# Kernel tuning notes

Measured on AMD Instinct MI355X. Metric: run time of the kernel, lower is better.

Reference implementation:

```python
import jax, jax.numpy as jnp
import numpy as np

B, S, E, H = 16, 512, 768, 12
D = E // H
SCALING = 1.0 / np.sqrt(D * 1.0)  # scaling_factor = 1


def setup_inputs() -> dict:
    key = jax.random.key(0)
    ks = jax.random.split(key, 8)
    query = jax.random.normal(ks[0], (B, S, E), dtype=jnp.float32)
    key_in = jax.random.normal(ks[1], (B, S, E), dtype=jnp.float32)
    value = jax.random.normal(ks[2], (B, S, E), dtype=jnp.float32)
    key_padding_mask = jax.random.randint(ks[3], (B, S), 0, 2).astype(jnp.bool_)
    attn_bias = jax.random.normal(ks[4], (B, H, S, S), dtype=jnp.float32)
    # Learned params. NOTE: original code applies wq to q, k AND v (wk/wv unused).
    Wq = jax.random.normal(ks[5], (E, E), dtype=jnp.float32) * (1.0 / np.sqrt(E))
    bq = jnp.zeros((E,), dtype=jnp.float32)
    Wo = jax.random.normal(ks[6], (E, E), dtype=jnp.float32) * (1.0 / np.sqrt(E))
    bo = jnp.zeros((E,), dtype=jnp.float32)
    return {"query": query, "key": key_in, "value": value,
            "key_padding_mask": key_padding_mask, "attn_bias": attn_bias,
            "Wq": Wq, "bq": bq, "Wo": Wo, "bo": bo}


def _split_heads(x):
    # [B,S,E] -> [B,H,S,D]
    return x.reshape(B, S, H, D).transpose(0, 2, 1, 3)


def reference(query, key, value, key_padding_mask, attn_bias, Wq, bq, Wo, bo):
    q = (query @ Wq + bq) * jnp.asarray(SCALING, query.dtype)
    k = key @ Wq + bq      # faithful: wq used for k and v in the source
    v = value @ Wq + bq
    q, k, v = _split_heads(q), _split_heads(k), _split_heads(v)  # [B,H,S,D]
    w = jnp.einsum('bhtd,bhsd->bhts', q, k)                      # [B,H,T,S]
    w = jnp.where(key_padding_mask[:, None, None, :], -jnp.inf, w)
    w = w + attn_bias
    attn = jax.nn.softmax(w, axis=-1)  # dropout is no-op (training=False)
    o = jnp.einsum('bhts,bhsd->bhtd', attn, v)
    o = o.transpose(0, 2, 1, 3).reshape(B, S, E)
    o = o @ Wo + bo
    attn_weights = w.reshape(B * H, S, S)
    return (o, attn_weights, attn.reshape(B * H, S, S))
```

## Files before the change

### kernel.cpp

```cpp
#include <hip/hip_runtime.h>
#include <cmath>

#define BB 16
#define SS 512
#define EE 768
#define HH 12
#define DD 64
#define NBH (BB*HH)

#define MASK_NEG (-1.0e30f)

__device__ __forceinline__ unsigned short bf16_rn(float x) {
    unsigned u = __float_as_uint(x);
    u += 0x7FFFu + ((u >> 16) & 1u);
    return (unsigned short)(u >> 16);
}
__device__ __forceinline__ float bf16_tof(unsigned short h) {
    return __uint_as_float(((unsigned)h) << 16);
}

typedef __attribute__((ext_vector_type(8))) short bf16x8;
typedef __attribute__((ext_vector_type(4))) float f32x4;
typedef __attribute__((ext_vector_type(4))) unsigned short u16x4;

__global__ __launch_bounds__(256) void conv_w_kernel(
    const float* __restrict__ Wq, const float* __restrict__ Wo,
    unsigned short* __restrict__ wtq, unsigned short* __restrict__ wto)
{
    const float* __restrict__ W = blockIdx.z ? Wo : Wq;
    unsigned short* __restrict__ wt = blockIdx.z ? wto : wtq;
    const int k = blockIdx.x * 256 + threadIdx.x;
    const int n = blockIdx.y;
    const float x = W[(size_t)k * EE + n];
    const unsigned short h = bf16_rn(x);
    const float r = x - bf16_tof(h);
    const unsigned short m = bf16_rn(r);
    const float l2 = r - bf16_tof(m);
    const unsigned short l = bf16_rn(l2);
    const size_t PL = (size_t)EE * EE;
    wt[0 * PL + (size_t)n * EE + k] = h;
    wt[1 * PL + (size_t)n * EE + k] = m;
    wt[2 * PL + (size_t)n * EE + k] = l;
}

__global__ __launch_bounds__(256) void split_gemm_qkv_kernel(
    const float* __restrict__ Xq, const float* __restrict__ Xk,
    const float* __restrict__ Xv, const unsigned short* __restrict__ wt,
    const float* __restrict__ bvec,
    unsigned short* __restrict__ qp, unsigned short* __restrict__ kp,
    unsigned short* __restrict__ vtp)
{
    const int z = blockIdx.z;
    const float* __restrict__ X = (z == 1) ? Xk : (z == 2) ? Xv : Xq;
    const float scale = (z == 0) ? 0.125f : 1.0f;

    const int m0 = blockIdx.x * 128;
    const int n0 = blockIdx.y * 128;

    __shared__ __align__(16) unsigned short lds[4 * 4096];
    const int AH = 0, AL = 4096, BH = 8192, BL = 12288;

    const int tid = threadIdx.x;
    const int srow = tid >> 2;
    const int sg   = tid & 3;
    const int wv = tid >> 6;
    const int wr = wv >> 1, wc = wv & 1;
    const int lane = tid & 63;
    const int l15 = lane & 15, lg = lane >> 4;

    const size_t PL = (size_t)EE * EE;
    const size_t PS = (size_t)NBH * SS * DD;

    f32x4 acc[4][4];
#pragma unroll
    for (int i = 0; i < 4; ++i)
#pragma unroll
        for (int j = 0; j < 4; ++j) acc[i][j] = (f32x4){0.f, 0.f, 0.f, 0.f};

    float4 xf[2][2];
    bf16x8 wh[2], wl[2];

#define QKV_LOAD(K0)                                                          \
    {                                                                         \
        _Pragma("unroll")                                                     \
        for (int half = 0; half < 2; ++half) {                                \
            const int row = srow + 64 * half;                                 \
            const float* xp = &X[(size_t)(m0 + row) * EE + (K0) + sg * 8];    \
            xf[half][0] = *reinterpret_cast<const float4*>(xp);               \
            xf[half][1] = *reinterpret_cast<const float4*>(xp + 4);           \
            const size_t bo = (size_t)(n0 + row) * EE + (K0) + sg * 8;        \
            wh[half] = *reinterpret_cast<const bf16x8*>(&wt[0 * PL + bo]);    \
            wl[half] = *reinterpret_cast<const bf16x8*>(&wt[1 * PL + bo]);    \
        }                                                                     \
    }

    QKV_LOAD(0);

#pragma unroll 1
    for (int k0 = 0; k0 < EE; k0 += 32) {
        __syncthreads();
#pragma unroll
        for (int half = 0; half < 2; ++half) {
            const int row = srow + 64 * half;
            const float xs[8] = {xf[half][0].x, xf[half][0].y, xf[half][0].z, xf[half][0].w,
                                 xf[half][1].x, xf[half][1].y, xf[half][1].z, xf[half][1].w};
            bf16x8 hv, mv;
#pragma unroll
            for (int e = 0; e < 8; ++e) {
                const float x = xs[e];
                const unsigned short h = bf16_rn(x);
                const unsigned short m = bf16_rn(x - bf16_tof(h));
                hv[e] = (short)h;
                mv[e] = (short)m;
            }
            const int o = row * 32 + sg * 8;
            *reinterpret_cast<bf16x8*>(&lds[AH + o]) = hv;
            *reinterpret_cast<bf16x8*>(&lds[AL + o]) = mv;
            *reinterpret_cast<bf16x8*>(&lds[BH + o]) = wh[half];
            *reinterpret_cast<bf16x8*>(&lds[BL + o]) = wl[half];
        }
        __syncthreads();

        if (k0 + 32 < EE) QKV_LOAD(k0 + 32);

        bf16x8 ah[4], al[4];
#pragma unroll
        for (int i = 0; i < 4; ++i) {
            const int o = (wr * 64 + i * 16 + l15) * 32 + lg * 8;
            ah[i] = *reinterpret_cast<const bf16x8*>(&lds[AH + o]);
            al[i] = *reinterpret_cast<const bf16x8*>(&lds[AL + o]);
        }
#pragma unroll
        for (int j = 0; j < 4; ++j) {
            const int o = (wc * 64 + j * 16 + l15) * 32 + lg * 8;
            const bf16x8 bh = *reinterpret_cast<const bf16x8*>(&lds[BH + o]);
            const bf16x8 bl = *reinterpret_cast<const bf16x8*>(&lds[BL + o]);
#pragma unroll
            for (int i = 0; i < 4; ++i) {
                acc[i][j] = __builtin_amdgcn_mfma_f32_16x16x32_bf16(ah[i], bh, acc[i][j], 0, 0, 0);
                acc[i][j] = __builtin_amdgcn_mfma_f32_16x16x32_bf16(ah[i], bl, acc[i][j], 0, 0, 0);
                acc[i][j] = __builtin_amdgcn_mfma_f32_16x16x32_bf16(al[i], bh, acc[i][j], 0, 0, 0);
                acc[i][j] = __builtin_amdgcn_mfma_f32_16x16x32_bf16(al[i], bl, acc[i][j], 0, 0, 0);
            }
        }
    }
#undef QKV_LOAD

    unsigned short* __restrict__ dstp = (z == 0) ? qp : kp;
#pragma unroll
    for (int j = 0; j < 4; ++j) {
        const int n = n0 + wc * 64 + j * 16 + l15;
        const float bvn = bvec[n];
        const int h = n >> 6, d = n & 63;
#pragma unroll
        for (int i = 0; i < 4; ++i) {
            const int mb = m0 + wr * 64 + i * 16 + lg * 4;
#pragma unroll
            for (int r = 0; r < 4; ++r) {
                const int m = mb + r;
                const int bh_ = (m >> 9) * HH + h;
                const int srow_ = m & 511;
                const float val = (acc[i][j][r] + bvn) * scale;
                const unsigned short hi = bf16_rn(val);
                const unsigned short lo = bf16_rn(val - bf16_tof(hi));
                if (z == 2) {
                    const size_t o = ((size_t)bh_ * DD + d) * SS + srow_;
                    vtp[o] = hi;
                    vtp[o + PS] = lo;
                } else {
                    const size_t o = ((size_t)bh_ * SS + srow_) * DD + d;
                    dstp[o] = hi;
                    dstp[o + PS] = lo;
                }
            }
        }
    }
}

__global__ __launch_bounds__(256) void flash_attn_kernel(
    const unsigned short* __restrict__ qp, const unsigned short* __restrict__ kp,
    const unsigned short* __restrict__ vt, const unsigned char* __restrict__ mask,
    const float* __restrict__ bias, float* __restrict__ wout,
    float* __restrict__ ohb, float* __restrict__ stat_m,
    float* __restrict__ stat_inv)
{
    const int p = blockIdx.x;
    const int g = p >> 3;
    const int bh = (p & 7) * 24 + (g >> 3);
    const int t0 = (g & 7) * 64;
    const int b = bh / HH, h = bh % HH;
    const int tid = threadIdx.x;
    const int wv = tid >> 6;
    const int lane = tid & 63, l15 = lane & 15, lg = lane >> 4;
    const size_t PS = (size_t)NBH * SS * DD;

    __shared__ __align__(16) unsigned short kbuf[2 * 64 * 68];
    __shared__ __align__(16) unsigned short vbuf[2 * 64 * 68];
    __shared__ __align__(16) unsigned short pbuf[4 * 2 * 16 * 68];

    bf16x8 bqh[2], bql[2];
    {
        const unsigned short* qbase = &qp[((size_t)bh * SS + t0 + wv * 16) * DD];
#pragma unroll
        for (int kc = 0; kc < 2; ++kc) {
            const size_t o = (size_t)l15 * DD + kc * 32 + lg * 8;
            bqh[kc] = *reinterpret_cast<const bf16x8*>(&qbase[o]);
            bql[kc] = *reinterpret_cast<const bf16x8*>(&qbase[o + PS]);
        }
    }

    float rm = -3.0e38f, rs = 0.0f;

    f32x4 oac[4];
#pragma unroll
    for (int j = 0; j < 4; ++j) oac[j] = (f32x4){0.f, 0.f, 0.f, 0.f};

    const int t = t0 + wv * 16 + l15;

    const unsigned short* __restrict__ kb0 = &kp[(size_t)bh * SS * DD];
    const unsigned short* __restrict__ vb0 = &vt[(size_t)bh * DD * SS];
    const int srow2 = tid >> 3, sg2 = (tid & 7) * 8;

    bf16x8 krh[2], krl[2], vrh[2], vrl[2];

#define FA_LOADKV(SC)                                                         \
    {                                                                         \
        _Pragma("unroll")                                                     \
        for (int rep = 0; rep < 2; ++rep) {                                   \
            const int row = srow2 + rep * 32;                                 \
            krh[rep] = *reinterpret_cast<const bf16x8*>(                      \
                &kb0[(size_t)((SC) + row) * DD + sg2]);                       \
            krl[rep] = *reinterpret_cast<const bf16x8*>(                      \
                &kb0[(size_t)((SC) + row) * DD + sg2 + PS]);                  \
            vrh[rep] = *reinterpret_cast<const bf16x8*>(                      \
                &vb0[(size_t)row * SS + (SC) + sg2]);                         \
            vrl[rep] = *reinterpret_cast<const bf16x8*>(                      \
                &vb0[(size_t)row * SS + (SC) + sg2 + PS]);                    \
        }                                                                     \
    }

    FA_LOADKV(0);

#pragma unroll 1
    for (int c = 0; c < 8; ++c) {
        const int sc = c * 64;
        __syncthreads();

#pragma unroll
        for (int rep = 0; rep < 2; ++rep) {
            const int row = srow2 + rep * 32;
            *reinterpret_cast<bf16x8*>(&kbuf[row * 68 + sg2]) = krh[rep];
            *reinterpret_cast<bf16x8*>(&kbuf[64 * 68 + row * 68 + sg2]) = krl[rep];
            *reinterpret_cast<bf16x8*>(&vbuf[row * 68 + sg2]) = vrh[rep];
            *reinterpret_cast<bf16x8*>(&vbuf[64 * 68 + row * 68 + sg2]) = vrl[rep];
        }
        __syncthreads();

        if (c < 7) FA_LOADKV(sc + 64);

        float4 bvr[4];
        uchar4 mkr[4];
#pragma unroll
        for (int i = 0; i < 4; ++i) {
            const int s = sc + i * 16 + lg * 4;
            bvr[i] = *reinterpret_cast<const float4*>(&bias[((size_t)bh * SS + t) * SS + s]);
            mkr[i] = *reinterpret_cast<const uchar4*>(&mask[b * SS + s]);
        }

        f32x4 ws[4];
#pragma unroll
        for (int i = 0; i < 4; ++i) ws[i] = (f32x4){0.f, 0.f, 0.f, 0.f};
#pragma unroll
        for (int kc = 0; kc < 2; ++kc) {
#pragma unroll
            for (int i = 0; i < 4; ++i) {
                const int o = (i * 16 + l15) * 68 + kc * 32 + lg * 8;
                const bf16x8 ah = *reinterpret_cast<const bf16x8*>(&kbuf[o]);
                const bf16x8 al = *reinterpret_cast<const bf16x8*>(&kbuf[64 * 68 + o]);
                ws[i] = __builtin_amdgcn_mfma_f32_16x16x32_bf16(ah, bqh[kc], ws[i], 0, 0, 0);
                ws[i] = __builtin_amdgcn_mfma_f32_16x16x32_bf16(ah, bql[kc], ws[i], 0, 0, 0);
                ws[i] = __builtin_amdgcn_mfma_f32_16x16x32_bf16(al, bqh[kc], ws[i], 0, 0, 0);
                ws[i] = __builtin_amdgcn_mfma_f32_16x16x32_bf16(al, bql[kc], ws[i], 0, 0, 0);
            }
        }

        float mx = -3.0e38f;
#pragma unroll
        for (int i = 0; i < 4; ++i) {
            const int s = sc + i * 16 + lg * 4;
            const size_t go = ((size_t)bh * SS + t) * SS + s;
            float4 w4;
            w4.x = mkr[i].x ? MASK_NEG : ws[i][0] + bvr[i].x;
            w4.y = mkr[i].y ? MASK_NEG : ws[i][1] + bvr[i].y;
            w4.z = mkr[i].z ? MASK_NEG : ws[i][2] + bvr[i].z;
            w4.w = mkr[i].w ? MASK_NEG : ws[i][3] + bvr[i].w;
            *reinterpret_cast<float4*>(&wout[go]) = w4;
            ws[i][0] = w4.x; ws[i][1] = w4.y; ws[i][2] = w4.z; ws[i][3] = w4.w;
            mx = fmaxf(mx, fmaxf(fmaxf(w4.x, w4.y), fmaxf(w4.z, w4.w)));
        }
        mx = fmaxf(mx, __shfl_xor(mx, 16));
        mx = fmaxf(mx, __shfl_xor(mx, 32));

        const float m_new = fmaxf(rm, mx);
        float sm = 0.0f;
#pragma unroll
        for (int i = 0; i < 4; ++i)
#pragma unroll
            for (int r = 0; r < 4; ++r) sm += __expf(ws[i][r] - m_new);
        sm += __shfl_xor(sm, 16);
        sm += __shfl_xor(sm, 32);
        const float scl = __expf(rm - m_new);
        rs = rs * scl + sm;
        rm = m_new;

        unsigned short* pw = &pbuf[(wv * 2) * 16 * 68];
#pragma unroll
        for (int i = 0; i < 4; ++i) {
            float4 p4;
            p4.x = __expf(ws[i][0] - m_new);
            p4.y = __expf(ws[i][1] - m_new);
            p4.z = __expf(ws[i][2] - m_new);
            p4.w = __expf(ws[i][3] - m_new);
            u16x4 hv, lv;
            hv.x = bf16_rn(p4.x); lv.x = bf16_rn(p4.x - bf16_tof(hv.x));
            hv.y = bf16_rn(p4.y); lv.y = bf16_rn(p4.y - bf16_tof(hv.y));
            hv.z = bf16_rn(p4.z); lv.z = bf16_rn(p4.z - bf16_tof(hv.z));
            hv.w = bf16_rn(p4.w); lv.w = bf16_rn(p4.w - bf16_tof(hv.w));
            const int po = l15 * 68 + i * 16 + lg * 4;
            *reinterpret_cast<u16x4*>(&pw[po]) = hv;
            *reinterpret_cast<u16x4*>(&pw[16 * 68 + po]) = lv;
        }

        float sclr[4];
#pragma unroll
        for (int r = 0; r < 4; ++r) sclr[r] = __shfl(scl, lg * 4 + r);
#pragma unroll
        for (int j = 0; j < 4; ++j)
#pragma unroll
            for (int r = 0; r < 4; ++r) oac[j][r] *= sclr[r];

#pragma unroll
        for (int kc = 0; kc < 2; ++kc) {
            const int ko = kc * 32 + lg * 8;
            const bf16x8 pah = *reinterpret_cast<const bf16x8*>(&pw[l15 * 68 + ko]);
            const bf16x8 pal = *reinterpret_cast<const bf16x8*>(&pw[16 * 68 + l15 * 68 + ko]);
#pragma unroll
            for (int j = 0; j < 4; ++j) {
                const int o = (j * 16 + l15) * 68 + ko;
                const bf16x8 vh = *reinterpret_cast<const bf16x8*>(&vbuf[o]);
                const bf16x8 vl = *reinterpret_cast<const bf16x8*>(&vbuf[64 * 68 + o]);
                oac[j] = __builtin_amdgcn_mfma_f32_16x16x32_bf16(pah, vh, oac[j], 0, 0, 0);
                oac[j] = __builtin_amdgcn_mfma_f32_16x16x32_bf16(pah, vl, oac[j], 0, 0, 0);
                oac[j] = __builtin_amdgcn_mfma_f32_16x16x32_bf16(pal, vh, oac[j], 0, 0, 0);
                oac[j] = __builtin_amdgcn_mfma_f32_16x16x32_bf16(pal, vl, oac[j], 0, 0, 0);
            }
        }
    }
#undef FA_LOADKV

    const float inv = 1.0f / rs;
    if (lg == 0) {
        stat_m[(size_t)bh * SS + t] = rm;
        stat_inv[(size_t)bh * SS + t] = inv;
    }
    float invr[4];
#pragma unroll
    for (int r = 0; r < 4; ++r) invr[r] = __shfl(inv, lg * 4 + r);
#pragma unroll
    for (int j = 0; j < 4; ++j)
#pragma unroll
        for (int r = 0; r < 4; ++r) {
            const int tr = t0 + wv * 16 + lg * 4 + r;
            ohb[((size_t)b * SS + tr) * EE + h * DD + j * 16 + l15] = oac[j][r] * invr[r];
        }
}

__global__ __launch_bounds__(256) void finish_kernel(
    const float* __restrict__ X, const unsigned short* __restrict__ wt,
    const float* __restrict__ bvec, float* __restrict__ dflat,
    const float* __restrict__ win, const float* __restrict__ stat_m,
    const float* __restrict__ stat_inv, float* __restrict__ attn)
{
    __shared__ __align__(16) unsigned short lds[4 * 4096];

    if (blockIdx.x >= 384) {
        const int nb = gridDim.x - 384;
        const size_t total = (size_t)NBH * SS * (SS / 4);
        for (size_t g = (size_t)(blockIdx.x - 384) * 256 + threadIdx.x; g < total;
             g += (size_t)nb * 256) {
            const size_t row = g >> 7;
            const float m_ = stat_m[row];
            const float iv = stat_inv[row];
            const float4 w4 = reinterpret_cast<const float4*>(win)[g];
            float4 p4;
            p4.x = __expf(w4.x - m_) * iv;
            p4.y = __expf(w4.y - m_) * iv;
            p4.z = __expf(w4.z - m_) * iv;
            p4.w = __expf(w4.w - m_) * iv;
            reinterpret_cast<float4*>(attn)[g] = p4;
        }
        return;
    }

    const int m0 = (blockIdx.x & 63) * 128;
    const int n0 = (blockIdx.x >> 6) * 128;

    const int AH = 0, AM = 4096, BH = 8192, BM = 12288;

    const int tid = threadIdx.x;
    const int srow = tid >> 2;
    const int sg   = tid & 3;
    const int wv = tid >> 6;
    const int wr = wv >> 1, wc = wv & 1;
    const int lane = tid & 63;
    const int l15 = lane & 15, lg = lane >> 4;
    const size_t PL = (size_t)EE * EE;

    f32x4 acc[4][4];
#pragma unroll
    for (int i = 0; i < 4; ++i)
#pragma unroll
        for (int j = 0; j < 4; ++j) acc[i][j] = (f32x4){0.f, 0.f, 0.f, 0.f};

#pragma unroll 1
    for (int k0 = 0; k0 < EE; k0 += 32) {
#pragma unroll
        for (int half = 0; half < 2; ++half) {
            const int row = srow + 64 * half;
            const float* xp = &X[(size_t)(m0 + row) * EE + k0 + sg * 8];
            const float4 f0 = *reinterpret_cast<const float4*>(xp);
            const float4 f1 = *reinterpret_cast<const float4*>(xp + 4);
            const float xs[8] = {f0.x, f0.y, f0.z, f0.w, f1.x, f1.y, f1.z, f1.w};
            bf16x8 hv, mv;
#pragma unroll
            for (int e = 0; e < 8; ++e) {
                const float x = xs[e];
                const unsigned short h = bf16_rn(x);
                const unsigned short m = bf16_rn(x - bf16_tof(h));
                hv[e] = (short)h;
                mv[e] = (short)m;
            }
            const int o = row * 32 + sg * 8;
            *reinterpret_cast<bf16x8*>(&lds[AH + o]) = hv;
            *reinterpret_cast<bf16x8*>(&lds[AM + o]) = mv;

            const size_t bo = (size_t)(n0 + row) * EE + k0 + sg * 8;
            *reinterpret_cast<bf16x8*>(&lds[BH + o]) =
                *reinterpret_cast<const bf16x8*>(&wt[0 * PL + bo]);
            *reinterpret_cast<bf16x8*>(&lds[BM + o]) =
                *reinterpret_cast<const bf16x8*>(&wt[1 * PL + bo]);
        }
        __syncthreads();

        bf16x8 ah[4], am[4];
#pragma unroll
        for (int i = 0; i < 4; ++i) {
            const int o = (wr * 64 + i * 16 + l15) * 32 + lg * 8;
            ah[i] = *reinterpret_cast<const bf16x8*>(&lds[AH + o]);
            am[i] = *reinterpret_cast<const bf16x8*>(&lds[AM + o]);
        }
#pragma unroll
        for (int j = 0; j < 4; ++j) {
            const int o = (wc * 64 + j * 16 + l15) * 32 + lg * 8;
            const bf16x8 bh = *reinterpret_cast<const bf16x8*>(&lds[BH + o]);
            const bf16x8 bm = *reinterpret_cast<const bf16x8*>(&lds[BM + o]);
#pragma unroll
            for (int i = 0; i < 4; ++i) {
                acc[i][j] = __builtin_amdgcn_mfma_f32_16x16x32_bf16(ah[i], bh, acc[i][j], 0, 0, 0);
                acc[i][j] = __builtin_amdgcn_mfma_f32_16x16x32_bf16(ah[i], bm, acc[i][j], 0, 0, 0);
                acc[i][j] = __builtin_amdgcn_mfma_f32_16x16x32_bf16(am[i], bh, acc[i][j], 0, 0, 0);
                acc[i][j] = __builtin_amdgcn_mfma_f32_16x16x32_bf16(am[i], bm, acc[i][j], 0, 0, 0);
            }
        }
        __syncthreads();
    }

#pragma unroll
    for (int j = 0; j < 4; ++j) {
        const int n = n0 + wc * 64 + j * 16 + l15;
        const float bvn = bvec[n];
#pragma unroll
        for (int i = 0; i < 4; ++i) {
            const int mb = m0 + wr * 64 + i * 16 + lg * 4;
#pragma unroll
            for (int r = 0; r < 4; ++r)
                dflat[(size_t)(mb + r) * EE + n] = acc[i][j][r] + bvn;
        }
    }
}

__global__ __launch_bounds__(256) void proj_kernel(
    const float* __restrict__ Xq, const float* __restrict__ Xk,
    const float* __restrict__ Xv, const float* __restrict__ W,
    const float* __restrict__ bvec, float* __restrict__ qb,
    float* __restrict__ kb, float* __restrict__ vb)
{
    const int z = blockIdx.z;
    const float* __restrict__ X = (z == 0) ? Xq : (z == 1) ? Xk : Xv;
    float* __restrict__ Dst = (z == 0) ? qb : (z == 1) ? kb : vb;
    const float scale = (z == 0) ? 0.125f : 1.0f;

    const int m0 = blockIdx.x * 128;
    const int n0 = blockIdx.y * 128;

    __shared__ float As[16][128];
    __shared__ float Bs[16][128];

    const int tid = threadIdx.x;
    const int ty = tid >> 4, tx = tid & 15;

    float acc[8][8];
#pragma unroll
    for (int i = 0; i < 8; ++i)
#pragma unroll
        for (int j = 0; j < 8; ++j) acc[i][j] = 0.0f;

    const int arow = tid >> 1;
    const int ak   = (tid & 1) * 8;
    const int brow = tid >> 4;
    const int bn   = (tid & 15) * 8;

    for (int k0 = 0; k0 < EE; k0 += 16) {
        const float4* ap = reinterpret_cast<const float4*>(&X[(size_t)(m0 + arow) * EE + k0 + ak]);
        float4 a0 = ap[0], a1 = ap[1];
        As[ak + 0][arow] = a0.x; As[ak + 1][arow] = a0.y;
        As[ak + 2][arow] = a0.z; As[ak + 3][arow] = a0.w;
        As[ak + 4][arow] = a1.x; As[ak + 5][arow] = a1.y;
        As[ak + 6][arow] = a1.z; As[ak + 7][arow] = a1.w;

        const float4* bp = reinterpret_cast<const float4*>(&W[(size_t)(k0 + brow) * EE + n0 + bn]);
        float4 b0 = bp[0], b1 = bp[1];
        *reinterpret_cast<float4*>(&Bs[brow][bn])     = b0;
        *reinterpret_cast<float4*>(&Bs[brow][bn + 4]) = b1;
        __syncthreads();

#pragma unroll
        for (int kk = 0; kk < 16; ++kk) {
            float4 aA = *reinterpret_cast<const float4*>(&As[kk][ty * 8]);
            float4 aB = *reinterpret_cast<const float4*>(&As[kk][ty * 8 + 4]);
            float4 bA = *reinterpret_cast<const float4*>(&Bs[kk][tx * 8]);
            float4 bB = *reinterpret_cast<const float4*>(&Bs[kk][tx * 8 + 4]);
            float av[8] = {aA.x, aA.y, aA.z, aA.w, aB.x, aB.y, aB.z, aB.w};
            float bv[8] = {bA.x, bA.y, bA.z, bA.w, bB.x, bB.y, bB.z, bB.w};
#pragma unroll
            for (int i = 0; i < 8; ++i)
#pragma unroll
                for (int j = 0; j < 8; ++j)
                    acc[i][j] = fmaf(av[i], bv[j], acc[i][j]);
        }
        __syncthreads();
    }

    const int nbase = n0 + tx * 8;
    float bq8[8];
    {
        float4 c0 = *reinterpret_cast<const float4*>(&bvec[nbase]);
        float4 c1 = *reinterpret_cast<const float4*>(&bvec[nbase + 4]);
        bq8[0]=c0.x; bq8[1]=c0.y; bq8[2]=c0.z; bq8[3]=c0.w;
        bq8[4]=c1.x; bq8[5]=c1.y; bq8[6]=c1.z; bq8[7]=c1.w;
    }
    const int hh = nbase >> 6;
    const int dd = nbase & 63;
#pragma unroll
    for (int i = 0; i < 8; ++i) {
        const int m = m0 + ty * 8 + i;
        const int bidx = m >> 9;
        const int srow = m & 511;
        float* dst = &Dst[(((size_t)bidx * HH + hh) * SS + srow) * DD + dd];
        float4 v0, v1;
        v0.x = (acc[i][0] + bq8[0]) * scale;
        v0.y = (acc[i][1] + bq8[1]) * scale;
        v0.z = (acc[i][2] + bq8[2]) * scale;
        v0.w = (acc[i][3] + bq8[3]) * scale;
        v1.x = (acc[i][4] + bq8[4]) * scale;
        v1.y = (acc[i][5] + bq8[5]) * scale;
        v1.z = (acc[i][6] + bq8[6]) * scale;
        v1.w = (acc[i][7] + bq8[7]) * scale;
        *reinterpret_cast<float4*>(dst)     = v0;
        *reinterpret_cast<float4*>(dst + 4) = v1;
    }
}

__global__ __launch_bounds__(256) void scores_kernel(
    const float* __restrict__ qb, const float* __restrict__ kb,
    const unsigned char* __restrict__ mask,
    const float* __restrict__ bias, float* __restrict__ wout)
{
    const int bh = blockIdx.z;
    const int b  = bh / HH;
    const int t0 = blockIdx.y * 128;
    const int s0 = blockIdx.x * 128;

    __shared__ float As[16][128];
    __shared__ float Bs[16][128];

    const int tid = threadIdx.x;
    const int ty = tid >> 4, tx = tid & 15;

    float acc[8][8];
#pragma unroll
    for (int i = 0; i < 8; ++i)
#pragma unroll
        for (int j = 0; j < 8; ++j) acc[i][j] = 0.0f;

    const int arow = tid >> 1;
    const int ak   = (tid & 1) * 8;

    const float* __restrict__ qbase = &qb[(size_t)bh * SS * DD];
    const float* __restrict__ kbase = &kb[(size_t)bh * SS * DD];

    for (int k0 = 0; k0 < DD; k0 += 16) {
        const float4* ap = reinterpret_cast<const float4*>(&qbase[(size_t)(t0 + arow) * DD + k0 + ak]);
        float4 a0 = ap[0], a1 = ap[1];
        As[ak + 0][arow] = a0.x; As[ak + 1][arow] = a0.y;
        As[ak + 2][arow] = a0.z; As[ak + 3][arow] = a0.w;
        As[ak + 4][arow] = a1.x; As[ak + 5][arow] = a1.y;
        As[ak + 6][arow] = a1.z; As[ak + 7][arow] = a1.w;

        const float4* bp = reinterpret_cast<const float4*>(&kbase[(size_t)(s0 + arow) * DD + k0 + ak]);
        float4 b0 = bp[0], b1 = bp[1];
        Bs[ak + 0][arow] = b0.x; Bs[ak + 1][arow] = b0.y;
        Bs[ak + 2][arow] = b0.z; Bs[ak + 3][arow] = b0.w;
        Bs[ak + 4][arow] = b1.x; Bs[ak + 5][arow] = b1.y;
        Bs[ak + 6][arow] = b1.z; Bs[ak + 7][arow] = b1.w;
        __syncthreads();

#pragma unroll
        for (int kk = 0; kk < 16; ++kk) {
            float4 aA = *reinterpret_cast<const float4*>(&As[kk][ty * 8]);
            float4 aB = *reinterpret_cast<const float4*>(&As[kk][ty * 8 + 4]);
            float4 bA = *reinterpret_cast<const float4*>(&Bs[kk][tx * 8]);
            float4 bB = *reinterpret_cast<const float4*>(&Bs[kk][tx * 8 + 4]);
            float av[8] = {aA.x, aA.y, aA.z, aA.w, aB.x, aB.y, aB.z, aB.w};
            float bv[8] = {bA.x, bA.y, bA.z, bA.w, bB.x, bB.y, bB.z, bB.w};
#pragma unroll
            for (int i = 0; i < 8; ++i)
#pragma unroll
                for (int j = 0; j < 8; ++j)
                    acc[i][j] = fmaf(av[i], bv[j], acc[i][j]);
        }
        __syncthreads();
    }

    const int scol = s0 + tx * 8;
    const uint2 mv = *reinterpret_cast<const uint2*>(&mask[b * SS + scol]);
    bool msk[8];
    msk[0] = (mv.x & 0x000000ffu) != 0;
    msk[1] = (mv.x & 0x0000ff00u) != 0;
    msk[2] = (mv.x & 0x00ff0000u) != 0;
    msk[3] = (mv.x & 0xff000000u) != 0;
    msk[4] = (mv.y & 0x000000ffu) != 0;
    msk[5] = (mv.y & 0x0000ff00u) != 0;
    msk[6] = (mv.y & 0x00ff0000u) != 0;
    msk[7] = (mv.y & 0xff000000u) != 0;
#pragma unroll
    for (int i = 0; i < 8; ++i) {
        const int t = t0 + ty * 8 + i;
        const float4 bv0 = *reinterpret_cast<const float4*>(&bias[((size_t)bh * SS + t) * SS + scol]);
        const float4 bv1 = *reinterpret_cast<const float4*>(&bias[((size_t)bh * SS + t) * SS + scol + 4]);
        float4 w0, w1;
        w0.x = msk[0] ? MASK_NEG : acc[i][0] + bv0.x;
        w0.y = msk[1] ? MASK_NEG : acc[i][1] + bv0.y;
        w0.z = msk[2] ? MASK_NEG : acc[i][2] + bv0.z;
        w0.w = msk[3] ? MASK_NEG : acc[i][3] + bv0.w;
        w1.x = msk[4] ? MASK_NEG : acc[i][4] + bv1.x;
        w1.y = msk[5] ? MASK_NEG : acc[i][5] + bv1.y;
        w1.z = msk[6] ? MASK_NEG : acc[i][6] + bv1.z;
        w1.w = msk[7] ? MASK_NEG : acc[i][7] + bv1.w;
        float* wrow = &wout[((size_t)bh * SS + t) * SS + scol];
        *reinterpret_cast<float4*>(wrow)     = w0;
        *reinterpret_cast<float4*>(wrow + 4) = w1;
    }
}

__global__ __launch_bounds__(256) void softmax_pv_kernel(
    const float* __restrict__ win, const float* __restrict__ vb,
    float* __restrict__ attn, float* __restrict__ ohb)
{
    const int bh = blockIdx.y;
    const int b = bh / HH, h = bh % HH;
    const int t0 = blockIdx.x * 64;
    const int wave = threadIdx.x >> 6;
    const int lane = threadIdx.x & 63;

    __shared__ float pws[4][8][512];

#pragma unroll 1
    for (int g = 0; g < 2; ++g) {
        const int tb = t0 + wave * 16 + g * 8;

#pragma unroll 1
        for (int r = 0; r < 8; ++r) {
            const int t = tb + r;
            const float4* wp = reinterpret_cast<const float4*>(&win[((size_t)bh * SS + t) * SS + lane * 8]);
            float4 w0 = wp[0], w1 = wp[1];
            float wv[8] = {w0.x,w0.y,w0.z,w0.w,w1.x,w1.y,w1.z,w1.w};
            float mx = wv[0];
#pragma unroll
            for (int j = 1; j < 8; ++j) mx = fmaxf(mx, wv[j]);
#pragma unroll
            for (int off = 32; off > 0; off >>= 1)
                mx = fmaxf(mx, __shfl_xor(mx, off));
            float e[8];
            float sum = 0.0f;
#pragma unroll
            for (int j = 0; j < 8; ++j) { e[j] = __expf(wv[j] - mx); sum += e[j]; }
#pragma unroll
            for (int off = 32; off > 0; off >>= 1)
                sum += __shfl_xor(sum, off);
            const float inv = 1.0f / sum;
            float4 p0, p1;
            p0.x = e[0]*inv; p0.y = e[1]*inv; p0.z = e[2]*inv; p0.w = e[3]*inv;
            p1.x = e[4]*inv; p1.y = e[5]*inv; p1.z = e[6]*inv; p1.w = e[7]*inv;
            float* arow = &attn[((size_t)bh * SS + t) * SS + lane * 8];
            *reinterpret_cast<float4*>(arow)     = p0;
            *reinterpret_cast<float4*>(arow + 4) = p1;
            *reinterpret_cast<float4*>(&pws[wave][r][lane * 8])     = p0;
            *reinterpret_cast<float4*>(&pws[wave][r][lane * 8 + 4]) = p1;
        }
        __syncthreads();

        float oacc[8] = {0,0,0,0,0,0,0,0};
#pragma unroll 2
        for (int s = 0; s < SS; s += 4) {
            const float v0 = vb[((size_t)bh * SS + s + 0) * DD + lane];
            const float v1 = vb[((size_t)bh * SS + s + 1) * DD + lane];
            const float v2 = vb[((size_t)bh * SS + s + 2) * DD + lane];
            const float v3 = vb[((size_t)bh * SS + s + 3) * DD + lane];
#pragma unroll
            for (int r = 0; r < 8; ++r) {
                const float4 p4 = *reinterpret_cast<const float4*>(&pws[wave][r][s]);
                oacc[r] = fmaf(p4.x, v0, oacc[r]);
                oacc[r] = fmaf(p4.y, v1, oacc[r]);
                oacc[r] = fmaf(p4.z, v2, oacc[r]);
                oacc[r] = fmaf(p4.w, v3, oacc[r]);
            }
        }
#pragma unroll
        for (int r = 0; r < 8; ++r)
            ohb[((size_t)b * SS + tb + r) * EE + h * DD + lane] = oacc[r];
        __syncthreads();
    }
}

__global__ __launch_bounds__(256) void outproj_kernel(
    const float* __restrict__ A, const float* __restrict__ W,
    const float* __restrict__ bvec, float* __restrict__ out)
{
    const int m0 = blockIdx.x * 128;
    const int n0 = blockIdx.y * 128;

    __shared__ float As[16][128];
    __shared__ float Bs[16][128];

    const int tid = threadIdx.x;
    const int ty = tid >> 4, tx = tid & 15;

    float acc[8][8];
#pragma unroll
    for (int i = 0; i < 8; ++i)
#pragma unroll
        for (int j = 0; j < 8; ++j) acc[i][j] = 0.0f;

    const int arow = tid >> 1;
    const int ak   = (tid & 1) * 8;
    const int brow = tid >> 4;
    const int bn   = (tid & 15) * 8;

    for (int k0 = 0; k0 < EE; k0 += 16) {
        const float4* ap = reinterpret_cast<const float4*>(&A[(size_t)(m0 + arow) * EE + k0 + ak]);
        float4 a0 = ap[0], a1 = ap[1];
        As[ak + 0][arow] = a0.x; As[ak + 1][arow] = a0.y;
        As[ak + 2][arow] = a0.z; As[ak + 3][arow] = a0.w;
        As[ak + 4][arow] = a1.x; As[ak + 5][arow] = a1.y;
        As[ak + 6][arow] = a1.z; As[ak + 7][arow] = a1.w;

        const float4* bp = reinterpret_cast<const float4*>(&W[(size_t)(k0 + brow) * EE + n0 + bn]);
        float4 b0 = bp[0], b1 = bp[1];
        *reinterpret_cast<float4*>(&Bs[brow][bn])     = b0;
        *reinterpret_cast<float4*>(&Bs[brow][bn + 4]) = b1;
        __syncthreads();

#pragma unroll
        for (int kk = 0; kk < 16; ++kk) {
            float4 aA = *reinterpret_cast<const float4*>(&As[kk][ty * 8]);
            float4 aB = *reinterpret_cast<const float4*>(&As[kk][ty * 8 + 4]);
            float4 bA = *reinterpret_cast<const float4*>(&Bs[kk][tx * 8]);
            float4 bB = *reinterpret_cast<const float4*>(&Bs[kk][tx * 8 + 4]);
            float av[8] = {aA.x, aA.y, aA.z, aA.w, aB.x, aB.y, aB.z, aB.w};
            float bv[8] = {bA.x, bA.y, bA.z, bA.w, bB.x, bB.y, bB.z, bB.w};
#pragma unroll
            for (int i = 0; i < 8; ++i)
#pragma unroll
                for (int j = 0; j < 8; ++j)
                    acc[i][j] = fmaf(av[i], bv[j], acc[i][j]);
        }
        __syncthreads();
    }

    const int nbase = n0 + tx * 8;
    float bq8[8];
    {
        float4 c0 = *reinterpret_cast<const float4*>(&bvec[nbase]);
        float4 c1 = *reinterpret_cast<const float4*>(&bvec[nbase + 4]);
        bq8[0]=c0.x; bq8[1]=c0.y; bq8[2]=c0.z; bq8[3]=c0.w;
        bq8[4]=c1.x; bq8[5]=c1.y; bq8[6]=c1.z; bq8[7]=c1.w;
    }
#pragma unroll
    for (int i = 0; i < 8; ++i) {
        const int m = m0 + ty * 8 + i;
        float* dst = &out[(size_t)m * EE + nbase];
        float4 v0, v1;
        v0.x = acc[i][0] + bq8[0]; v0.y = acc[i][1] + bq8[1];
        v0.z = acc[i][2] + bq8[2]; v0.w = acc[i][3] + bq8[3];
        v1.x = acc[i][4] + bq8[4]; v1.y = acc[i][5] + bq8[5];
        v1.z = acc[i][6] + bq8[6]; v1.w = acc[i][7] + bq8[7];
        *reinterpret_cast<float4*>(dst)     = v0;
        *reinterpret_cast<float4*>(dst + 4) = v1;
    }
}

extern "C" void kernel_launch(void* const* d_in, const int* in_sizes, int n_in,
                              void* d_out, int out_size, void* d_ws, size_t ws_size,
                              hipStream_t stream)
{
    const float* query = (const float*)d_in[0];
    const float* key   = (const float*)d_in[1];
    const float* value = (const float*)d_in[2];
    const unsigned char* mask = (const unsigned char*)d_in[3];
    const float* bias  = (const float*)d_in[4];
    const float* Wq    = (const float*)d_in[5];
    const float* bq    = (const float*)d_in[6];
    const float* Wo    = (const float*)d_in[7];
    const float* bo    = (const float*)d_in[8];

    float* out_o = (float*)d_out;
    float* out_w = out_o + (size_t)BB * SS * EE;
    float* out_a = out_w + (size_t)NBH * SS * SS;

    const size_t headsz = (size_t)NBH * SS * DD;
    const size_t wt_elems = 3 * (size_t)EE * EE;

    const size_t need_mfma = 3 * (2 * headsz * sizeof(unsigned short))
                           + headsz * sizeof(float)
                           + 2 * wt_elems * sizeof(unsigned short);

    if (ws_size >= need_mfma) {
        unsigned short* qp = (unsigned short*)d_ws;
        unsigned short* kp = qp + 2 * headsz;
        unsigned short* vt = kp + 2 * headsz;
        float* ohb = (float*)(vt + 2 * headsz);
        unsigned short* wtq = (unsigned short*)(ohb + headsz);
        unsigned short* wto = wtq + wt_elems;
        float* stat_m   = (float*)wtq;
        float* stat_inv = stat_m + (size_t)NBH * SS;

        conv_w_kernel<<<dim3(3, EE, 2), 256, 0, stream>>>(Wq, Wo, wtq, wto);
        split_gemm_qkv_kernel<<<dim3(64, 6, 3), 256, 0, stream>>>(
            query, key, value, wtq, bq, qp, kp, vt);
        flash_attn_kernel<<<dim3(8 * NBH), 256, 0, stream>>>(
            qp, kp, vt, mask, bias, out_w, ohb, stat_m, stat_inv);
        finish_kernel<<<384 + 2048, 256, 0, stream>>>(
            ohb, wto, bo, out_o, out_w, stat_m, stat_inv, out_a);
    } else {
        const size_t base_bytes = 4 * headsz * sizeof(float);
        if (ws_size < base_bytes) return;
        float* qb  = (float*)d_ws;
        float* kb  = qb + headsz;
        float* vb  = kb + headsz;
        float* ohb = vb + headsz;
        proj_kernel<<<dim3(64, 6, 3), 256, 0, stream>>>(query, key, value, Wq, bq, qb, kb, vb);
        scores_kernel<<<dim3(4, 4, NBH), 256, 0, stream>>>(qb, kb, mask, bias, out_w);
        softmax_pv_kernel<<<dim3(8, NBH), 256, 0, stream>>>(out_w, vb, out_a, ohb);
        outproj_kernel<<<dim3(64, 6), 256, 0, stream>>>(ohb, Wo, bo, out_o);
    }
}
```

Measured before the change: 438.9 us.

## Prefetch next K tile in out-projection GEMM and remap blocks for XCD locality

```diff
diff --git a/kernel.cpp b/kernel.cpp
--- a/kernel.cpp
+++ b/kernel.cpp
@@ -50,12 +50,15 @@
     unsigned short* __restrict__ qp, unsigned short* __restrict__ kp,
     unsigned short* __restrict__ vtp)
 {
-    const int z = blockIdx.z;
+    const int p = blockIdx.x;
+    const int z = p / 384;
+    const int q = p % 384;
+    const int xcd = q & 7, idx = q >> 3;
+    const int m0 = (xcd * 8 + (idx & 7)) * 128;
+    const int n0 = (idx >> 3) * 128;
+
     const float* __restrict__ X = (z == 1) ? Xk : (z == 2) ? Xv : Xq;
     const float scale = (z == 0) ? 0.125f : 1.0f;
-
-    const int m0 = blockIdx.x * 128;
-    const int n0 = blockIdx.y * 128;
 
     __shared__ __align__(16) unsigned short lds[4 * 4096];
     const int AH = 0, AL = 4096, BH = 8192, BL = 12288;
@@ -402,8 +405,10 @@
         return;
     }
 
-    const int m0 = (blockIdx.x & 63) * 128;
-    const int n0 = (blockIdx.x >> 6) * 128;
+    const int q = blockIdx.x;
+    const int xcd = q & 7, idx = q >> 3;
+    const int m0 = (xcd * 8 + (idx & 7)) * 128;
+    const int n0 = (idx >> 3) * 128;
 
     const int AH = 0, AM = 4096, BH = 8192, BM = 12288;
 
@@ -422,15 +427,33 @@
 #pragma unroll
         for (int j = 0; j < 4; ++j) acc[i][j] = (f32x4){0.f, 0.f, 0.f, 0.f};
 
+    float4 xf[2][2];
+    bf16x8 wh[2], wl[2];
+
+#define FIN_LOAD(K0)                                                          \
+    {                                                                         \
+        _Pragma("unroll")                                                     \
+        for (int half = 0; half < 2; ++half) {                                \
+            const int row = srow + 64 * half;                                 \
+            const float* xp = &X[(size_t)(m0 + row) * EE + (K0) + sg * 8];    \
+            xf[half][0] = *reinterpret_cast<const float4*>(xp);               \
+            xf[half][1] = *reinterpret_cast<const float4*>(xp + 4);           \
+            const size_t bo = (size_t)(n0 + row) * EE + (K0) + sg * 8;        \
+            wh[half] = *reinterpret_cast<const bf16x8*>(&wt[0 * PL + bo]);    \
+            wl[half] = *reinterpret_cast<const bf16x8*>(&wt[1 * PL + bo]);    \
+        }                                                                     \
+    }
+
+    FIN_LOAD(0);
+
 #pragma unroll 1
     for (int k0 = 0; k0 < EE; k0 += 32) {
+        __syncthreads();
 #pragma unroll
         for (int half = 0; half < 2; ++half) {
             const int row = srow + 64 * half;
-            const float* xp = &X[(size_t)(m0 + row) * EE + k0 + sg * 8];
-            const float4 f0 = *reinterpret_cast<const float4*>(xp);
-            const float4 f1 = *reinterpret_cast<const float4*>(xp + 4);
-            const float xs[8] = {f0.x, f0.y, f0.z, f0.w, f1.x, f1.y, f1.z, f1.w};
+            const float xs[8] = {xf[half][0].x, xf[half][0].y, xf[half][0].z, xf[half][0].w,
+                                 xf[half][1].x, xf[half][1].y, xf[half][1].z, xf[half][1].w};
             bf16x8 hv, mv;
 #pragma unroll
             for (int e = 0; e < 8; ++e) {
@@ -443,14 +466,12 @@
             const int o = row * 32 + sg * 8;
             *reinterpret_cast<bf16x8*>(&lds[AH + o]) = hv;
             *reinterpret_cast<bf16x8*>(&lds[AM + o]) = mv;
-
-            const size_t bo = (size_t)(n0 + row) * EE + k0 + sg * 8;
-            *reinterpret_cast<bf16x8*>(&lds[BH + o]) =
-                *reinterpret_cast<const bf16x8*>(&wt[0 * PL + bo]);
-            *reinterpret_cast<bf16x8*>(&lds[BM + o]) =
-                *reinterpret_cast<const bf16x8*>(&wt[1 * PL + bo]);
-        }
-        __syncthreads();
+            *reinterpret_cast<bf16x8*>(&lds[BH + o]) = wh[half];
+            *reinterpret_cast<bf16x8*>(&lds[BM + o]) = wl[half];
+        }
+        __syncthreads();
+
+        if (k0 + 32 < EE) FIN_LOAD(k0 + 32);
 
         bf16x8 ah[4], am[4];
 #pragma unroll
@@ -472,8 +493,8 @@
                 acc[i][j] = __builtin_amdgcn_mfma_f32_16x16x32_bf16(am[i], bm, acc[i][j], 0, 0, 0);
             }
         }
-        __syncthreads();
-    }
+    }
+#undef FIN_LOAD
 
 #pragma unroll
     for (int j = 0; j < 4; ++j) {
@@ -856,7 +877,7 @@
         float* stat_inv = stat_m + (size_t)NBH * SS;
 
         conv_w_kernel<<<dim3(3, EE, 2), 256, 0, stream>>>(Wq, Wo, wtq, wto);
-        split_gemm_qkv_kernel<<<dim3(64, 6, 3), 256, 0, stream>>>(
+        split_gemm_qkv_kernel<<<dim3(3 * 384), 256, 0, stream>>>(
             query, key, value, wtq, bq, qp, kp, vt);
         flash_attn_kernel<<<dim3(8 * NBH), 256, 0, stream>>>(
             qp, kp, vt, mask, bias, out_w, ohb, stat_m, stat_inv);
```

New measurement: 435.5 us. No clear change (-0.8%).
